# Kernel optimization log

Hardware: AMD Instinct MI355X
Metric: run time of the kernel (lower is better)

The kernel has to match this reference:

```python
import jax, jax.numpy as jnp
import numpy as np

NUM_GRIDS = 16
IN_X, IN_Z, OUT, BATCH = 32, 32, 64, 512


def _borders_cdf_grid(n_chunks):
    def inv_cdf(u):
        return np.log(2.0 * u) if u <= 0.5 else -np.log(2.0 * (1.0 - u))
    cs = 1.0 / n_chunks
    b = [inv_cdf(i * cs) for i in range(1, n_chunks)]
    left = b[0] - (b[1] - b[0])
    right = b[-1] + (b[-1] - b[-2])
    return np.array([left] + b + [right], dtype=np.float32)


def _laplace_cdf(v):
    e = jnp.exp(-jnp.abs(v))
    return jnp.where(v > 0, 1.0 - 0.5 * e, 0.5 * e)


def setup_inputs() -> dict:
    key = jax.random.key(0)
    k1, k2, k3 = jax.random.split(key, 3)
    scale = 0.1 / np.sqrt(IN_X * IN_Z)
    borders_np = _borders_cdf_grid(NUM_GRIDS)
    inv_len_np = (1.0 / (borders_np[1:] - borders_np[:-1])).astype(np.float32)
    return {
        "x": jax.random.normal(k1, (IN_X, BATCH), dtype=jnp.float32),
        "z": jax.random.normal(k2, (IN_Z, BATCH), dtype=jnp.float32),
        "func_parameter": jax.random.uniform(
            k3, (NUM_GRIDS + 1, NUM_GRIDS + 1, OUT, IN_X, IN_Z),
            dtype=jnp.float32, minval=-scale, maxval=scale),
        "borders": jnp.asarray(borders_np),
        "inverse_chunk_lengths": jnp.asarray(inv_len_np[:NUM_GRIDS]),
    }


def reference(x, z, func_parameter, borders, inverse_chunk_lengths):
    G = inverse_chunk_lengths.shape[0]
    Ix, B = x.shape
    Iz = z.shape[0]

    # data-dependent bin indices per (input_dim, batch) element
    idx_x = jnp.clip((_laplace_cdf(x) * G).astype(jnp.int32), 0, G - 1)  # [Ix,B]
    idx_z = jnp.clip((_laplace_cdf(z) * G).astype(jnp.int32), 0, G - 1)  # [Iz,B]
    dx = (x - borders[idx_x]) * inverse_chunk_lengths[idx_x]             # [Ix,B]
    dz = (z - borders[idx_z]) * inverse_chunk_lengths[idx_z]             # [Iz,B]
    idx_xn = jnp.clip(idx_x + 1, 0, G)
    idx_zn = jnp.clip(idx_z + 1, 0, G)

    # [Ix, Iz, G+1, G+1, O] so the per-(ix,iz) tables are leading-indexed
    Pt = jnp.transpose(func_parameter, (3, 4, 0, 1, 2))
    ax = jnp.arange(Ix)[:, None, None]   # [Ix,1,1]
    az = jnp.arange(Iz)[None, :, None]   # [1,Iz,1]

    def corner(ii, jj):  # ii:[Ix,1,B] or broadcastable, jj:[1,Iz,B]
        return Pt[ax, az, ii, jj]        # -> [Ix,Iz,B,O]

    ixb, ixnb = idx_x[:, None, :], idx_xn[:, None, :]
    izb, iznb = idx_z[None, :, :], idx_zn[None, :, :]
    wx, wz = dx[:, None, :], dz[None, :, :]             # [Ix,1,B],[1,Iz,B]

    out = (
        jnp.einsum('xzb,xzbo->ob', (1 - wx) * (1 - wz), corner(ixb, izb))
        + jnp.einsum('xzb,xzbo->ob', (1 - wx) * wz, corner(ixb, iznb))
        + jnp.einsum('xzb,xzbo->ob', wx * (1 - wz), corner(ixnb, izb))
        + jnp.einsum('xzb,xzbo->ob', wx * wz, corner(ixnb, iznb))
    )
    return out  # [output_dim, batch]
```

## Files before the change

### kernel.cpp

```cpp
#include <hip/hip_runtime.h>


#define NG        16
#define NB        17
#define IN_X      32
#define IN_Z      32
#define OUT_DIM   64
#define BATCH     512
#define CELLS     (NB * NB)
#define CSTRIDE   133
#define ILSTRIDE  33
#define XSTR_A    (NB * CSTRIDE)
#define STASKS    (CELLS * 32)

__device__ __forceinline__ void grid_coord(float v,
                                           const float* __restrict__ borders,
                                           const float* __restrict__ inv_len,
                                           int& idx, float& w) {
    float e   = expf(-fabsf(v));
    float cdf = (v > 0.f) ? (1.f - 0.5f * e) : (0.5f * e);
    int t = (int)(cdf * 16.f);
    t = t < 0 ? 0 : (t > NG - 1 ? NG - 1 : t);
    idx = t;
    w = (v - borders[t]) * inv_len[t];
}

__device__ __forceinline__ unsigned pack_bf16(float a, float b) {
    unsigned ua = __float_as_uint(a);
    unsigned ub = __float_as_uint(b);
    ua += 0x7FFFu + ((ua >> 16) & 1u);
    ub += 0x7FFFu + ((ub >> 16) & 1u);
    return (ua >> 16) | (ub & 0xFFFF0000u);
}
__device__ __forceinline__ float bf_lo(unsigned u) {
    return __uint_as_float(u << 16);
}
__device__ __forceinline__ float bf_hi(unsigned u) {
    return __uint_as_float(u & 0xFFFF0000u);
}

__global__ void precompute_kernel(const float* __restrict__ x,
                                  const float* __restrict__ z,
                                  const float* __restrict__ borders,
                                  const float* __restrict__ inv_len,
                                  float2* __restrict__ xc,
                                  uint2* __restrict__ zc,
                                  float* __restrict__ out) {
    const int gid = blockIdx.x * blockDim.x + threadIdx.x;
    out[gid] = 0.f;
    int idx; float w;
    if (gid < IN_X * BATCH) {
        grid_coord(x[gid], borders, inv_len, idx, w);
        xc[gid] = make_float2(w, __int_as_float(idx * XSTR_A));
    } else {
        const int g = gid - IN_X * BATCH;
        grid_coord(z[g], borders, inv_len, idx, w);
        zc[g] = make_uint2(__float_as_uint(w), (unsigned)(idx * CSTRIDE));
    }
}

__global__ __launch_bounds__(1024, 1)
void bf2d_kernel(const float2* __restrict__ xc,
                 const uint2* __restrict__ zc,
                 const float* __restrict__ P,
                 float* __restrict__ out) {
    __shared__ unsigned lds[CELLS * CSTRIDE];

    const int tid = threadIdx.x;
    const int op  = blockIdx.x & 31;
    const int iq  = blockIdx.x >> 5;
    const int o0  = op * 2;

    const float* Pb = P + (size_t)o0 * 1024 + iq * 128;
    #pragma unroll
    for (int it = 0; it < 10; ++it) {
        const int k = tid + it * 1024;
        if (k < STASKS) {
            const int c  = k >> 5;
            const int f4 = k & 31;
            const float* g = Pb + (size_t)c * 65536 + f4 * 4;
            const float4 a = *(const float4*)g;
            const float4 b = *(const float4*)(g + 1024);
            unsigned* d = &lds[c * CSTRIDE + (f4 >> 3) * ILSTRIDE
                               + ((f4 & 7) << 2)];
            d[0] = pack_bf16(a.x, b.x);
            d[1] = pack_bf16(a.y, b.y);
            d[2] = pack_bf16(a.z, b.z);
            d[3] = pack_bf16(a.w, b.w);
        }
    }
    __syncthreads();

    const int b  = tid & (BATCH - 1);
    const int ih = tid >> 9;
    const int il0 = 2 * ih, il1 = 2 * ih + 1;

    const float2 x0 = xc[(iq * 4 + il0) * BATCH + b];
    const float2 x1 = xc[(iq * 4 + il1) * BATCH + b];
    const float wx0 = x0.x, wx1 = x1.x;
    const int   xo0 = __float_as_int(x0.y) + il0 * ILSTRIDE;
    const int   xo1 = __float_as_int(x1.y) + il1 * ILSTRIDE;

    const uint2* zp = zc + b;
    float accx = 0.f, accy = 0.f;
    #pragma unroll 4
    for (int j = 0; j < IN_Z; ++j) {
        const uint2 zv = zp[j * BATCH];
        const float wz = __uint_as_float(zv.x);
        const int   zo = (int)zv.y + j;
        {
            const int base = xo0 + zo;
            const unsigned a0 = lds[base];
            const unsigned a1 = lds[base + CSTRIDE];
            const unsigned b0 = lds[base + XSTR_A];
            const unsigned b1 = lds[base + XSTR_A + CSTRIDE];
            const float lox = bf_lo(a0) + wz * (bf_lo(a1) - bf_lo(a0));
            const float loy = bf_hi(a0) + wz * (bf_hi(a1) - bf_hi(a0));
            const float hix = bf_lo(b0) + wz * (bf_lo(b1) - bf_lo(b0));
            const float hiy = bf_hi(b0) + wz * (bf_hi(b1) - bf_hi(b0));
            accx += lox + wx0 * (hix - lox);
            accy += loy + wx0 * (hiy - loy);
        }
        {
            const int base = xo1 + zo;
            const unsigned a0 = lds[base];
            const unsigned a1 = lds[base + CSTRIDE];
            const unsigned b0 = lds[base + XSTR_A];
            const unsigned b1 = lds[base + XSTR_A + CSTRIDE];
            const float lox = bf_lo(a0) + wz * (bf_lo(a1) - bf_lo(a0));
            const float loy = bf_hi(a0) + wz * (bf_hi(a1) - bf_hi(a0));
            const float hix = bf_lo(b0) + wz * (bf_lo(b1) - bf_lo(b0));
            const float hiy = bf_hi(b0) + wz * (bf_hi(b1) - bf_hi(b0));
            accx += lox + wx1 * (hix - lox);
            accy += loy + wx1 * (hiy - loy);
        }
    }

    atomicAdd(&out[o0 * BATCH + b],       accx);
    atomicAdd(&out[(o0 + 1) * BATCH + b], accy);
}

extern "C" void kernel_launch(void* const* d_in, const int* in_sizes, int n_in,
                              void* d_out, int out_size, void* d_ws, size_t ws_size,
                              hipStream_t stream) {
    const float* x       = (const float*)d_in[0];
    const float* z       = (const float*)d_in[1];
    const float* P       = (const float*)d_in[2];
    const float* borders = (const float*)d_in[3];
    const float* inv_len = (const float*)d_in[4];
    float* out = (float*)d_out;

    float2* xc = (float2*)d_ws;
    uint2*  zc = (uint2*)(xc + IN_X * BATCH);

    precompute_kernel<<<dim3(128), dim3(256), 0, stream>>>(
        x, z, borders, inv_len, xc, zc, out);

    bf2d_kernel<<<dim3(32 * 8), dim3(1024), 0, stream>>>(xc, zc, P, out);
}
```

Baseline: 123.2 us.

## Warp-specialize staging and compute with progress flags and sorted x-row ordering

Splits the block into 512 producer threads that stream P into LDS with register double-buffered prefetch and publish per-wave progress counters, and 512 consumer threads that each handle one batch element across all 4 x-rows. Consumers sort their 8 x-grid-row keys and wait only until the rows they need have been staged, so compute overlaps with the LDS fill instead of waiting at a full barrier. This adds spin-waiting on volatile shared flags, halves the threads doing compute, and relies on a row-to-progress mapping that must be exact for correctness.

```diff
diff --git a/kernel.cpp b/kernel.cpp
--- a/kernel.cpp
+++ b/kernel.cpp
@@ -12,6 +12,8 @@
 #define ILSTRIDE  33
 #define XSTR_A    (NB * CSTRIDE)
 #define STASKS    (CELLS * 32)
+#define NSTAGE    512
+#define NITER     19
 
 __device__ __forceinline__ void grid_coord(float v,
                                            const float* __restrict__ borders,
@@ -51,7 +53,7 @@
     int idx; float w;
     if (gid < IN_X * BATCH) {
         grid_coord(x[gid], borders, inv_len, idx, w);
-        xc[gid] = make_float2(w, __int_as_float(idx * XSTR_A));
+        xc[gid] = make_float2(w, __int_as_float(idx));
     } else {
         const int g = gid - IN_X * BATCH;
         grid_coord(z[g], borders, inv_len, idx, w);
@@ -65,74 +67,150 @@
                  const float* __restrict__ P,
                  float* __restrict__ out) {
     __shared__ unsigned lds[CELLS * CSTRIDE];
+    __shared__ unsigned prog[8];
 
     const int tid = threadIdx.x;
     const int op  = blockIdx.x & 31;
     const int iq  = blockIdx.x >> 5;
     const int o0  = op * 2;
 
-    const float* Pb = P + (size_t)o0 * 1024 + iq * 128;
-    #pragma unroll
-    for (int it = 0; it < 10; ++it) {
-        const int k = tid + it * 1024;
-        if (k < STASKS) {
-            const int c  = k >> 5;
-            const int f4 = k & 31;
-            const float* g = Pb + (size_t)c * 65536 + f4 * 4;
-            const float4 a = *(const float4*)g;
-            const float4 b = *(const float4*)(g + 1024);
-            unsigned* d = &lds[c * CSTRIDE + (f4 >> 3) * ILSTRIDE
-                               + ((f4 & 7) << 2)];
-            d[0] = pack_bf16(a.x, b.x);
-            d[1] = pack_bf16(a.y, b.y);
-            d[2] = pack_bf16(a.z, b.z);
-            d[3] = pack_bf16(a.w, b.w);
-        }
+    if (tid < 8) prog[tid] = 0u;
+    __syncthreads();
+
+    if (tid < NSTAGE) {
+        const int wv = tid >> 6;
+        volatile unsigned* vprog = prog;
+        const float* Pb = P + (size_t)o0 * 1024 + iq * 128;
+
+        float4 a0v, b0v, a1v, b1v;
+        {
+            const float* g0 = Pb + (size_t)(tid >> 5) * 65536 + (tid & 31) * 4;
+            a0v = *(const float4*)g0;
+            b0v = *(const float4*)(g0 + 1024);
+            const int k1 = tid + NSTAGE;
+            const float* g1 = Pb + (size_t)(k1 >> 5) * 65536 + (k1 & 31) * 4;
+            a1v = *(const float4*)g1;
+            b1v = *(const float4*)(g1 + 1024);
+        }
+        for (int it = 0; it < NITER; ++it) {
+            float4 a2v = make_float4(0.f, 0.f, 0.f, 0.f);
+            float4 b2v = a2v;
+            const int kp = tid + (it + 2) * NSTAGE;
+            if (kp < STASKS) {
+                const float* gp = Pb + (size_t)(kp >> 5) * 65536 + (kp & 31) * 4;
+                a2v = *(const float4*)gp;
+                b2v = *(const float4*)(gp + 1024);
+            }
+            const int k = tid + it * NSTAGE;
+            if (k < STASKS) {
+                const int c  = k >> 5;
+                const int f4 = k & 31;
+                unsigned* d = &lds[c * CSTRIDE + (f4 >> 3) * ILSTRIDE
+                                   + ((f4 & 7) << 2)];
+                d[0] = pack_bf16(a0v.x, b0v.x);
+                d[1] = pack_bf16(a0v.y, b0v.y);
+                d[2] = pack_bf16(a0v.z, b0v.z);
+                d[3] = pack_bf16(a0v.w, b0v.w);
+            }
+            asm volatile("s_waitcnt lgkmcnt(0)" ::: "memory");
+            if ((tid & 63) == 0) vprog[wv] = (unsigned)(it + 1);
+            a0v = a1v; b0v = b1v;
+            a1v = a2v; b1v = b2v;
+        }
+        return;
     }
-    __syncthreads();
-
-    const int b  = tid & (BATCH - 1);
-    const int ih = tid >> 9;
-    const int il0 = 2 * ih, il1 = 2 * ih + 1;
-
-    const float2 x0 = xc[(iq * 4 + il0) * BATCH + b];
-    const float2 x1 = xc[(iq * 4 + il1) * BATCH + b];
-    const float wx0 = x0.x, wx1 = x1.x;
-    const int   xo0 = __float_as_int(x0.y) + il0 * ILSTRIDE;
-    const int   xo1 = __float_as_int(x1.y) + il1 * ILSTRIDE;
-
+
+    const int b = tid - NSTAGE;
+    const float2 xv0 = xc[(iq * 4 + 0) * BATCH + b];
+    const float2 xv1 = xc[(iq * 4 + 1) * BATCH + b];
+    const float2 xv2 = xc[(iq * 4 + 2) * BATCH + b];
+    const float2 xv3 = xc[(iq * 4 + 3) * BATCH + b];
+    const float wx0 = xv0.x, wx1 = xv1.x, wx2 = xv2.x, wx3 = xv3.x;
+    const unsigned g0 = (unsigned)__float_as_int(xv0.y);
+    const unsigned g1 = (unsigned)__float_as_int(xv1.y);
+    const unsigned g2 = (unsigned)__float_as_int(xv2.y);
+    const unsigned g3 = (unsigned)__float_as_int(xv3.y);
+
+    unsigned key[8];
+    key[0] = (g0 << 3) | 0u;  key[1] = ((g0 + 1u) << 3) | 1u;
+    key[2] = (g1 << 3) | 2u;  key[3] = ((g1 + 1u) << 3) | 3u;
+    key[4] = (g2 << 3) | 4u;  key[5] = ((g2 + 1u) << 3) | 5u;
+    key[6] = (g3 << 3) | 6u;  key[7] = ((g3 + 1u) << 3) | 7u;
+
+#define CE(i, j) { const unsigned lo_ = key[i] < key[j] ? key[i] : key[j];   \
+                   const unsigned hi_ = key[i] < key[j] ? key[j] : key[i];   \
+                   key[i] = lo_; key[j] = hi_; }
+    CE(0,1) CE(2,3) CE(4,5) CE(6,7)
+    CE(0,2) CE(1,3) CE(4,6) CE(5,7)
+    CE(1,2) CE(5,6)
+    CE(0,4) CE(1,5) CE(2,6) CE(3,7)
+    CE(2,4) CE(3,5)
+    CE(1,2) CE(3,4) CE(5,6)
+#undef CE
+
+    volatile unsigned* vprog = prog;
     const uint2* zp = zc + b;
     float accx = 0.f, accy = 0.f;
-    #pragma unroll 4
-    for (int j = 0; j < IN_Z; ++j) {
-        const uint2 zv = zp[j * BATCH];
-        const float wz = __uint_as_float(zv.x);
-        const int   zo = (int)zv.y + j;
-        {
-            const int base = xo0 + zo;
-            const unsigned a0 = lds[base];
-            const unsigned a1 = lds[base + CSTRIDE];
-            const unsigned b0 = lds[base + XSTR_A];
-            const unsigned b1 = lds[base + XSTR_A + CSTRIDE];
-            const float lox = bf_lo(a0) + wz * (bf_lo(a1) - bf_lo(a0));
-            const float loy = bf_hi(a0) + wz * (bf_hi(a1) - bf_hi(a0));
-            const float hix = bf_lo(b0) + wz * (bf_lo(b1) - bf_lo(b0));
-            const float hiy = bf_hi(b0) + wz * (bf_hi(b1) - bf_hi(b0));
-            accx += lox + wx0 * (hix - lox);
-            accy += loy + wx0 * (hiy - loy);
-        }
-        {
-            const int base = xo1 + zo;
-            const unsigned a0 = lds[base];
-            const unsigned a1 = lds[base + CSTRIDE];
-            const unsigned b0 = lds[base + XSTR_A];
-            const unsigned b1 = lds[base + XSTR_A + CSTRIDE];
-            const float lox = bf_lo(a0) + wz * (bf_lo(a1) - bf_lo(a0));
-            const float loy = bf_hi(a0) + wz * (bf_hi(a1) - bf_hi(a0));
-            const float hix = bf_lo(b0) + wz * (bf_lo(b1) - bf_lo(b0));
-            const float hiy = bf_hi(b0) + wz * (bf_hi(b1) - bf_hi(b0));
-            accx += lox + wx1 * (hix - lox);
-            accy += loy + wx1 * (hiy - loy);
+    unsigned rows_done = 0;
+
+#pragma unroll
+    for (int ph = 0; ph < 4; ++ph) {
+        const unsigned kA = key[2 * ph], kB = key[2 * ph + 1];
+
+        int mx = (int)kB;
+#pragma unroll
+        for (int off = 32; off > 0; off >>= 1) {
+            const int o = __shfl_xor(mx, off);
+            mx = mx > o ? mx : o;
+        }
+        const unsigned need = (((unsigned)mx) >> 3) + 1u;
+        if (rows_done < need) {
+            for (;;) {
+                unsigned m = vprog[0];
+#pragma unroll
+                for (int w2 = 1; w2 < 8; ++w2) {
+                    const unsigned pv = vprog[w2];
+                    m = pv < m ? pv : m;
+                }
+                rows_done = (m * 16u) / 17u;
+                if (rows_done >= need) break;
+                __builtin_amdgcn_s_sleep(2);
+            }
+            asm volatile("" ::: "memory");
+        }
+
+        const unsigned nA = kA >> 3, nB = kB >> 3;
+        const int ilA = (int)((kA >> 1) & 3u), ilB = (int)((kB >> 1) & 3u);
+        const float wxA = ilA == 0 ? wx0 : ilA == 1 ? wx1 : ilA == 2 ? wx2 : wx3;
+        const float wxB = ilB == 0 ? wx0 : ilB == 1 ? wx1 : ilB == 2 ? wx2 : wx3;
+        const float wA = (kA & 1u) ? wxA : 1.f - wxA;
+        const float wB = (kB & 1u) ? wxB : 1.f - wxB;
+        const int baseA = (int)nA * XSTR_A + ilA * ILSTRIDE;
+        const int baseB = (int)nB * XSTR_A + ilB * ILSTRIDE;
+
+#pragma unroll 4
+        for (int j = 0; j < IN_Z; ++j) {
+            const uint2 zv = zp[j * BATCH];
+            const float wz = __uint_as_float(zv.x);
+            const int   zo = (int)zv.y + j;
+            {
+                const int ba = baseA + zo;
+                const unsigned q0 = lds[ba];
+                const unsigned q1 = lds[ba + CSTRIDE];
+                const float lx = bf_lo(q0) + wz * (bf_lo(q1) - bf_lo(q0));
+                const float ly = bf_hi(q0) + wz * (bf_hi(q1) - bf_hi(q0));
+                accx = fmaf(wA, lx, accx);
+                accy = fmaf(wA, ly, accy);
+            }
+            {
+                const int bb = baseB + zo;
+                const unsigned q0 = lds[bb];
+                const unsigned q1 = lds[bb + CSTRIDE];
+                const float lx = bf_lo(q0) + wz * (bf_lo(q1) - bf_lo(q0));
+                const float ly = bf_hi(q0) + wz * (bf_hi(q1) - bf_hi(q0));
+                accx = fmaf(wB, lx, accx);
+                accy = fmaf(wB, ly, accy);
+            }
         }
     }
 
```

Result: slower. 128.8 us (+4.5%).
